# Kernel optimization log

Hardware: AMD Instinct MI355X
Metric: run time of the kernel (lower is better)

The kernel has to match this reference:

```python
import jax, jax.numpy as jnp
import numpy as np

NUM_CLASSES = 1000
FEATURE_DIM = 1024
BATCH = 8192
MOMENTUM = 0.9
LAMBDA_INTRA = 1.0
LAMBDA_INTER = 0.5


def setup_inputs() -> dict:
    key = jax.random.key(0)
    k1, k2, k3, k4 = jax.random.split(key, 4)
    return {
        "features": jax.random.normal(k1, (BATCH, FEATURE_DIM), jnp.float32),
        "features_adv": jax.random.normal(k2, (BATCH, FEATURE_DIM), jnp.float32),
        "centers": jax.random.normal(k3, (NUM_CLASSES, FEATURE_DIM), jnp.float32),
        "labels": jax.random.randint(k4, (BATCH,), 0, NUM_CLASSES, dtype=jnp.int64),
    }


def _l2_normalize(x):
    # torch F.normalize(p=2, dim=1) with eps=1e-12 clamp on the norm
    n = jnp.linalg.norm(x, axis=1, keepdims=True)
    return x / jnp.maximum(n, 1e-12)


def _update_centers(centers, feats, labels):
    # Vectorized version of the per-class masked-mean momentum update.
    C = centers.shape[0]
    sums = jax.ops.segment_sum(feats, labels, num_segments=C)            # [C, D]
    counts = jax.ops.segment_sum(jnp.ones((feats.shape[0],), feats.dtype), labels, num_segments=C)  # [C]
    means = sums / jnp.maximum(counts, 1.0)[:, None]
    has_samples = (counts > 0)[:, None]
    center_is_zero = jnp.all(centers == 0, axis=1, keepdims=True)
    updated = jnp.where(center_is_zero, means, MOMENTUM * centers + (1.0 - MOMENTUM) * means)
    return jnp.where(has_samples, updated, centers)


def reference(features, features_adv, centers, labels):
    f = _l2_normalize(features)
    fa = _l2_normalize(features_adv)

    # update_centers runs under no_grad on detached normalized features
    centers_new = _update_centers(centers, jax.lax.stop_gradient(f), labels)

    centers_batch = centers_new[labels]  # [B, D] gather
    intra_clean = jnp.linalg.norm(f - centers_batch, axis=1).mean()
    intra_adv = jnp.linalg.norm(fa - centers_batch, axis=1).mean()

    # fused pairwise center distances: ||ci||^2 + ||cj||^2 - 2 ci.cj
    sq = jnp.sum(centers_new * centers_new, axis=1)                      # [C]
    d2 = sq[:, None] + sq[None, :] - 2.0 * (centers_new @ centers_new.T)  # [C, C]
    dist = jnp.sqrt(jnp.maximum(d2, 0.0))
    C = centers_new.shape[0]
    upper = jnp.triu(jnp.ones((C, C), dtype=bool), k=1)
    n_pairs = C * (C - 1) / 2.0
    inter_loss = jnp.sum(jnp.where(upper, jax.nn.relu(1.0 - dist), 0.0)) / n_pairs

    return LAMBDA_INTRA * (intra_clean + intra_adv) - LAMBDA_INTER * inter_loss
```

## Files before the change

### kernel.cpp

```cpp
#include <hip/hip_runtime.h>
#include <math.h>

#define BATCH 8192
#define DIM 1024
#define NCLS 1000
#define NPAD 1024
#define NPAIRS 499500.0f

typedef float  f32x4  __attribute__((ext_vector_type(4)));
typedef short  bf16x8 __attribute__((ext_vector_type(8)));


__device__ inline float waveAllReduceAdd(float x) {
  #pragma unroll
  for (int m = 32; m > 0; m >>= 1) x += __shfl_xor(x, m);
  return x;
}

__device__ inline float blockReduce1(float x, float* sm) {
  x = waveAllReduceAdd(x);
  int lane = threadIdx.x & 63, wid = threadIdx.x >> 6;
  __syncthreads();
  if (lane == 0) sm[wid] = x;
  __syncthreads();
  return sm[0] + sm[1] + sm[2] + sm[3];
}

__device__ inline float bf2f(unsigned short u) {
  return __uint_as_float(((unsigned int)u) << 16);
}

__device__ inline unsigned short f2bf(float f) {
  unsigned int u = __float_as_uint(f);
  u += 0x7FFFu + ((u >> 16) & 1u);
  return (unsigned short)(u >> 16);
}


__global__ void zero_kernel(int* counts, float* partials) {
  int t = threadIdx.x;
  if (t < NCLS) counts[t] = 0;
  if (t < 768) partials[t] = 0.0f;
}

__global__ void norms_count_kernel(const float* __restrict__ feats,
                                   const int* __restrict__ labels,
                                   float* __restrict__ invn, int* counts) {
  int lane = threadIdx.x & 63;
  int row = blockIdx.x * 4 + (threadIdx.x >> 6);
  const float4* f4 = (const float4*)(feats + (size_t)row * DIM);
  float ss = 0.f;
  #pragma unroll
  for (int i = 0; i < 4; ++i) {
    float4 v = f4[lane + 64 * i];
    ss += v.x * v.x + v.y * v.y + v.z * v.z + v.w * v.w;
  }
  ss = waveAllReduceAdd(ss);
  if (lane == 0) {
    invn[row] = 1.0f / fmaxf(sqrtf(ss), 1e-12f);
    atomicAdd(&counts[labels[row]], 1);
  }
}

__global__ void scan_kernel(const int* __restrict__ counts, int* offsets, int* cursor) {
  __shared__ int s[1024];
  int t = threadIdx.x;
  int v = (t < NCLS) ? counts[t] : 0;
  s[t] = v;
  __syncthreads();
  for (int off = 1; off < 1024; off <<= 1) {
    int u = (t >= off) ? s[t - off] : 0;
    __syncthreads();
    s[t] += u;
    __syncthreads();
  }
  if (t < NCLS) {
    int e = s[t] - v;
    offsets[t] = e;
    cursor[t] = e;
  }
}

__global__ void scatter_kernel(const int* __restrict__ labels, int* cursor,
                               int* rows_sorted) {
  int j = blockIdx.x * 256 + threadIdx.x;
  if (j < BATCH) {
    int pos = atomicAdd(&cursor[labels[j]], 1);
    rows_sorted[pos] = j;
  }
}


__global__ void update_centers_kernel(const float* __restrict__ feats,
                                      const float* __restrict__ centers,
                                      const int* __restrict__ counts,
                                      const int* __restrict__ offsets,
                                      const int* __restrict__ rows_sorted,
                                      const float* __restrict__ invn,
                                      unsigned short* __restrict__ centers_bf,
                                      float* __restrict__ sqn) {
  __shared__ float sm[8];
  __shared__ int s_anynz;
  int c = blockIdx.x;
  int tid = threadIdx.x;

  if (c >= NCLS) {
    ushort4 z = make_ushort4(0, 0, 0, 0);
    ((ushort4*)(centers_bf + (size_t)c * DIM))[tid] = z;
    return;
  }

  int n = counts[c];
  int off = offsets[c];

  float4 acc = make_float4(0.f, 0.f, 0.f, 0.f);
  for (int t = 0; t < n; ++t) {
    int r = rows_sorted[off + t];
    float w = invn[r];
    float4 v = ((const float4*)(feats + (size_t)r * DIM))[tid];
    acc.x += v.x * w; acc.y += v.y * w; acc.z += v.z * w; acc.w += v.w * w;
  }

  float invc = 1.0f / fmaxf((float)n, 1.0f);
  float4 mean = make_float4(acc.x * invc, acc.y * invc, acc.z * invc, acc.w * invc);

  float4 cv = ((const float4*)(centers + (size_t)c * DIM))[tid];
  if (tid == 0) s_anynz = 0;
  __syncthreads();
  if (cv.x != 0.f || cv.y != 0.f || cv.z != 0.f || cv.w != 0.f) s_anynz = 1;
  __syncthreads();

  float4 o;
  if (s_anynz) {
    o = make_float4(0.9f * cv.x + 0.1f * mean.x, 0.9f * cv.y + 0.1f * mean.y,
                    0.9f * cv.z + 0.1f * mean.z, 0.9f * cv.w + 0.1f * mean.w);
  } else {
    o = mean;
  }
  if (n == 0) o = cv;

  ushort4 ob = make_ushort4(f2bf(o.x), f2bf(o.y), f2bf(o.z), f2bf(o.w));
  ((ushort4*)(centers_bf + (size_t)c * DIM))[tid] = ob;

  float sq = blockReduce1(o.x * o.x + o.y * o.y + o.z * o.z + o.w * o.w, sm);
  if (tid == 0) sqn[c] = sq;
}


__global__ void intra_kernel(const float* __restrict__ feats,
                             const float* __restrict__ featsa,
                             const unsigned short* __restrict__ centers_bf,
                             const int* __restrict__ labels,
                             const float* __restrict__ invn,
                             float* __restrict__ partials) {
  int lane = threadIdx.x & 63;
  int row = blockIdx.x * 4 + (threadIdx.x >> 6);
  const float4* f4 = (const float4*)(feats + (size_t)row * DIM);
  const float4* a4 = (const float4*)(featsa + (size_t)row * DIM);
  int lab = labels[row];
  const ushort4* c4 = (const ushort4*)(centers_bf + (size_t)lab * DIM);

  float4 fv[4], av[4];
  ushort4 cv[4];
  float ssa = 0.f;
  #pragma unroll
  for (int i = 0; i < 4; ++i) {
    fv[i] = f4[lane + 64 * i];
    av[i] = a4[lane + 64 * i];
    cv[i] = c4[lane + 64 * i];
    ssa += av[i].x * av[i].x + av[i].y * av[i].y + av[i].z * av[i].z + av[i].w * av[i].w;
  }
  ssa = waveAllReduceAdd(ssa);
  float inva = 1.0f / fmaxf(sqrtf(ssa), 1e-12f);
  float invf = invn[row];

  float d2c = 0.f, d2a = 0.f;
  #pragma unroll
  for (int i = 0; i < 4; ++i) {
    float cx = bf2f(cv[i].x), cy = bf2f(cv[i].y), cz = bf2f(cv[i].z), cw = bf2f(cv[i].w);
    float dx = fv[i].x * invf - cx, dy = fv[i].y * invf - cy;
    float dz = fv[i].z * invf - cz, dw = fv[i].w * invf - cw;
    d2c += dx * dx + dy * dy + dz * dz + dw * dw;
    float ex = av[i].x * inva - cx, ey = av[i].y * inva - cy;
    float ez = av[i].z * inva - cz, ew = av[i].w * inva - cw;
    d2a += ex * ex + ey * ey + ez * ez + ew * ew;
  }
  d2c = waveAllReduceAdd(d2c);
  d2a = waveAllReduceAdd(d2a);
  if (lane == 0) {
    int slot = row & 255;
    atomicAdd(&partials[slot], sqrtf(d2c));
    atomicAdd(&partials[256 + slot], sqrtf(d2a));
  }
}


__global__ void inter_mfma_kernel(const unsigned short* __restrict__ Cbf,
                                  const float* __restrict__ sq,
                                  float* __restrict__ inter_partial) {
  int bi = blockIdx.y, bj = blockIdx.x;
  if (bj < bi) return;

  __shared__ float smr[8];
  int tid = threadIdx.x;
  int w = tid >> 6;
  int wy = w >> 1, wx = w & 1;
  int lane = tid & 63;
  int m = lane & 15;
  int q = lane >> 4;

  int i0 = bi * 64 + wy * 32;
  int j0 = bj * 64 + wx * 32;

  const unsigned short* arow0 = Cbf + (size_t)(i0 + m) * DIM;
  const unsigned short* arow1 = Cbf + (size_t)(i0 + 16 + m) * DIM;
  const unsigned short* brow0 = Cbf + (size_t)(j0 + m) * DIM;
  const unsigned short* brow1 = Cbf + (size_t)(j0 + 16 + m) * DIM;

  f32x4 acc00 = {0.f, 0.f, 0.f, 0.f}, acc01 = acc00, acc10 = acc00, acc11 = acc00;

  #pragma unroll 4
  for (int k0 = 0; k0 < DIM; k0 += 32) {
    int ko = k0 + q * 8;
    bf16x8 a0 = *(const bf16x8*)(arow0 + ko);
    bf16x8 a1 = *(const bf16x8*)(arow1 + ko);
    bf16x8 b0 = *(const bf16x8*)(brow0 + ko);
    bf16x8 b1 = *(const bf16x8*)(brow1 + ko);
    acc00 = __builtin_amdgcn_mfma_f32_16x16x32_bf16(a0, b0, acc00, 0, 0, 0);
    acc01 = __builtin_amdgcn_mfma_f32_16x16x32_bf16(a0, b1, acc01, 0, 0, 0);
    acc10 = __builtin_amdgcn_mfma_f32_16x16x32_bf16(a1, b0, acc10, 0, 0, 0);
    acc11 = __builtin_amdgcn_mfma_f32_16x16x32_bf16(a1, b1, acc11, 0, 0, 0);
  }

  float local = 0.f;
  int colA = lane & 15;
  int rbase = (lane >> 4) * 4;
  #pragma unroll
  for (int si = 0; si < 2; ++si) {
    #pragma unroll
    for (int sj = 0; sj < 2; ++sj) {
      f32x4 a = (si == 0) ? (sj == 0 ? acc00 : acc01) : (sj == 0 ? acc10 : acc11);
      #pragma unroll
      for (int r = 0; r < 4; ++r) {
        int i = i0 + si * 16 + rbase + r;
        int j = j0 + sj * 16 + colA;
        if (j < NCLS && i < j) {
          float d2 = sq[i] + sq[j] - 2.0f * a[r];
          float d = sqrtf(fmaxf(d2, 0.0f));
          local += fmaxf(1.0f - d, 0.0f);
        }
      }
    }
  }
  float tot = blockReduce1(local, smr);
  if (tid == 0) atomicAdd(&inter_partial[(bi * 16 + bj) & 255], tot);
}


__global__ void final_kernel(const float* __restrict__ partials, float* __restrict__ out) {
  __shared__ float sm[8];
  int t = threadIdx.x;
  float c = partials[t] + partials[256 + t];
  float e = partials[512 + t];
  c = blockReduce1(c, sm);
  e = blockReduce1(e, sm);
  if (t == 0) {
    float intra = c * (1.0f / (float)BATCH);
    float inter = e / NPAIRS;
    out[0] = intra - 0.5f * inter;
  }
}


extern "C" void kernel_launch(void* const* d_in, const int* in_sizes, int n_in,
                              void* d_out, int out_size, void* d_ws, size_t ws_size,
                              hipStream_t stream) {
  const float* features     = (const float*)d_in[0];
  const float* features_adv = (const float*)d_in[1];
  const float* centers      = (const float*)d_in[2];
  const int*   labels       = (const int*)d_in[3];
  float* out = (float*)d_out;

  unsigned short* centers_bf = (unsigned short*)d_ws;
  float* sqn = (float*)(centers_bf + (size_t)NPAD * DIM);
  float* invn = sqn + NCLS;
  float* partials = invn + BATCH;
  int* counts = (int*)(partials + 768);
  int* offsets = counts + NCLS;
  int* cursor = offsets + NCLS;
  int* rows_sorted = cursor + NCLS;

  hipLaunchKernelGGL(zero_kernel, dim3(1), dim3(1024), 0, stream, counts, partials);
  hipLaunchKernelGGL(norms_count_kernel, dim3(BATCH / 4), dim3(256), 0, stream,
                     features, labels, invn, counts);
  hipLaunchKernelGGL(scan_kernel, dim3(1), dim3(1024), 0, stream, counts, offsets, cursor);
  hipLaunchKernelGGL(scatter_kernel, dim3(BATCH / 256), dim3(256), 0, stream, labels,
                     cursor, rows_sorted);
  hipLaunchKernelGGL(update_centers_kernel, dim3(NPAD), dim3(256), 0, stream, features,
                     centers, counts, offsets, rows_sorted, invn, centers_bf, sqn);
  hipLaunchKernelGGL(intra_kernel, dim3(BATCH / 4), dim3(256), 0, stream, features,
                     features_adv, centers_bf, labels, invn, partials);
  hipLaunchKernelGGL(inter_mfma_kernel, dim3(16, 16), dim3(256), 0, stream, centers_bf,
                     sqn, partials + 512);
  hipLaunchKernelGGL(final_kernel, dim3(1), dim3(256), 0, stream, partials, out);
}
```

Measured before the change: 155.1 us.

## Fuse intra-class distance into per-class center update and merge histogram with scan

Merges the zero, label-count and prefix-scan kernels into a single block that builds the histogram in shared memory. The intra-distance kernel is folded into the per-class update kernel: each class block re-reads its samples' clean and adversarial rows and computes distances against the fp32 updated center kept in registers. This removes two launches and the bf16 center gather, but each class block now walks its samples serially with three block-wide reductions (several barriers) per sample. The fused phase also runs at per-class granularity over 1000 blocks, so load imbalance across classes is possible.

```diff
diff --git a/kernel.cpp b/kernel.cpp
--- a/kernel.cpp
+++ b/kernel.cpp
@@ -26,6 +26,16 @@
   return sm[0] + sm[1] + sm[2] + sm[3];
 }
 
+__device__ inline float2 blockReduce2(float x, float y, float* sm) {
+  x = waveAllReduceAdd(x);
+  y = waveAllReduceAdd(y);
+  int lane = threadIdx.x & 63, wid = threadIdx.x >> 6;
+  __syncthreads();
+  if (lane == 0) { sm[wid * 2] = x; sm[wid * 2 + 1] = y; }
+  __syncthreads();
+  return make_float2(sm[0] + sm[2] + sm[4] + sm[6], sm[1] + sm[3] + sm[5] + sm[7]);
+}
+
 __device__ inline float bf2f(unsigned short u) {
   return __uint_as_float(((unsigned int)u) << 16);
 }
@@ -37,15 +47,7 @@
 }
 
 
-__global__ void zero_kernel(int* counts, float* partials) {
-  int t = threadIdx.x;
-  if (t < NCLS) counts[t] = 0;
-  if (t < 768) partials[t] = 0.0f;
-}
-
-__global__ void norms_count_kernel(const float* __restrict__ feats,
-                                   const int* __restrict__ labels,
-                                   float* __restrict__ invn, int* counts) {
+__global__ void norms_kernel(const float* __restrict__ feats, float* __restrict__ invn) {
   int lane = threadIdx.x & 63;
   int row = blockIdx.x * 4 + (threadIdx.x >> 6);
   const float4* f4 = (const float4*)(feats + (size_t)row * DIM);
@@ -56,30 +58,35 @@
     ss += v.x * v.x + v.y * v.y + v.z * v.z + v.w * v.w;
   }
   ss = waveAllReduceAdd(ss);
-  if (lane == 0) {
-    invn[row] = 1.0f / fmaxf(sqrtf(ss), 1e-12f);
-    atomicAdd(&counts[labels[row]], 1);
-  }
-}
-
-__global__ void scan_kernel(const int* __restrict__ counts, int* offsets, int* cursor) {
-  __shared__ int s[1024];
+  if (lane == 0) invn[row] = 1.0f / fmaxf(sqrtf(ss), 1e-12f);
+}
+
+
+__global__ void hist_scan_kernel(const int* __restrict__ labels, int* counts,
+                                 int* offsets, int* cursor, float* partials) {
+  __shared__ int h[1024];
   int t = threadIdx.x;
-  int v = (t < NCLS) ? counts[t] : 0;
-  s[t] = v;
-  __syncthreads();
+  h[t] = 0;
+  if (t < 768) partials[t] = 0.0f;
+  __syncthreads();
+  #pragma unroll
+  for (int j = t; j < BATCH; j += 1024) atomicAdd(&h[labels[j]], 1);
+  __syncthreads();
+  int v = h[t];
+  if (t < NCLS) counts[t] = v;
   for (int off = 1; off < 1024; off <<= 1) {
-    int u = (t >= off) ? s[t - off] : 0;
+    int u = (t >= off) ? h[t - off] : 0;
     __syncthreads();
-    s[t] += u;
+    h[t] += u;
     __syncthreads();
   }
   if (t < NCLS) {
-    int e = s[t] - v;
+    int e = h[t] - v;
     offsets[t] = e;
     cursor[t] = e;
   }
 }
+
 
 __global__ void scatter_kernel(const int* __restrict__ labels, int* cursor,
                                int* rows_sorted) {
@@ -91,22 +98,23 @@
 }
 
 
-__global__ void update_centers_kernel(const float* __restrict__ feats,
-                                      const float* __restrict__ centers,
-                                      const int* __restrict__ counts,
-                                      const int* __restrict__ offsets,
-                                      const int* __restrict__ rows_sorted,
-                                      const float* __restrict__ invn,
-                                      unsigned short* __restrict__ centers_bf,
-                                      float* __restrict__ sqn) {
+__global__ void update_intra_kernel(const float* __restrict__ feats,
+                                    const float* __restrict__ featsa,
+                                    const float* __restrict__ centers,
+                                    const int* __restrict__ counts,
+                                    const int* __restrict__ offsets,
+                                    const int* __restrict__ rows_sorted,
+                                    const float* __restrict__ invn,
+                                    unsigned short* __restrict__ centers_bf,
+                                    float* __restrict__ sqn,
+                                    float* __restrict__ partials) {
   __shared__ float sm[8];
   __shared__ int s_anynz;
   int c = blockIdx.x;
   int tid = threadIdx.x;
 
   if (c >= NCLS) {
-    ushort4 z = make_ushort4(0, 0, 0, 0);
-    ((ushort4*)(centers_bf + (size_t)c * DIM))[tid] = z;
+    ((ushort4*)(centers_bf + (size_t)c * DIM))[tid] = make_ushort4(0, 0, 0, 0);
     return;
   }
 
@@ -120,7 +128,6 @@
     float4 v = ((const float4*)(feats + (size_t)r * DIM))[tid];
     acc.x += v.x * w; acc.y += v.y * w; acc.z += v.z * w; acc.w += v.w * w;
   }
-
   float invc = 1.0f / fmaxf((float)n, 1.0f);
   float4 mean = make_float4(acc.x * invc, acc.y * invc, acc.z * invc, acc.w * invc);
 
@@ -139,58 +146,33 @@
   }
   if (n == 0) o = cv;
 
-  ushort4 ob = make_ushort4(f2bf(o.x), f2bf(o.y), f2bf(o.z), f2bf(o.w));
-  ((ushort4*)(centers_bf + (size_t)c * DIM))[tid] = ob;
+  ((ushort4*)(centers_bf + (size_t)c * DIM))[tid] =
+      make_ushort4(f2bf(o.x), f2bf(o.y), f2bf(o.z), f2bf(o.w));
 
   float sq = blockReduce1(o.x * o.x + o.y * o.y + o.z * o.z + o.w * o.w, sm);
   if (tid == 0) sqn[c] = sq;
-}
-
-
-__global__ void intra_kernel(const float* __restrict__ feats,
-                             const float* __restrict__ featsa,
-                             const unsigned short* __restrict__ centers_bf,
-                             const int* __restrict__ labels,
-                             const float* __restrict__ invn,
-                             float* __restrict__ partials) {
-  int lane = threadIdx.x & 63;
-  int row = blockIdx.x * 4 + (threadIdx.x >> 6);
-  const float4* f4 = (const float4*)(feats + (size_t)row * DIM);
-  const float4* a4 = (const float4*)(featsa + (size_t)row * DIM);
-  int lab = labels[row];
-  const ushort4* c4 = (const ushort4*)(centers_bf + (size_t)lab * DIM);
-
-  float4 fv[4], av[4];
-  ushort4 cv[4];
-  float ssa = 0.f;
-  #pragma unroll
-  for (int i = 0; i < 4; ++i) {
-    fv[i] = f4[lane + 64 * i];
-    av[i] = a4[lane + 64 * i];
-    cv[i] = c4[lane + 64 * i];
-    ssa += av[i].x * av[i].x + av[i].y * av[i].y + av[i].z * av[i].z + av[i].w * av[i].w;
-  }
-  ssa = waveAllReduceAdd(ssa);
-  float inva = 1.0f / fmaxf(sqrtf(ssa), 1e-12f);
-  float invf = invn[row];
-
-  float d2c = 0.f, d2a = 0.f;
-  #pragma unroll
-  for (int i = 0; i < 4; ++i) {
-    float cx = bf2f(cv[i].x), cy = bf2f(cv[i].y), cz = bf2f(cv[i].z), cw = bf2f(cv[i].w);
-    float dx = fv[i].x * invf - cx, dy = fv[i].y * invf - cy;
-    float dz = fv[i].z * invf - cz, dw = fv[i].w * invf - cw;
-    d2c += dx * dx + dy * dy + dz * dz + dw * dw;
-    float ex = av[i].x * inva - cx, ey = av[i].y * inva - cy;
-    float ez = av[i].z * inva - cz, ew = av[i].w * inva - cw;
-    d2a += ex * ex + ey * ey + ez * ez + ew * ew;
-  }
-  d2c = waveAllReduceAdd(d2c);
-  d2a = waveAllReduceAdd(d2a);
-  if (lane == 0) {
-    int slot = row & 255;
-    atomicAdd(&partials[slot], sqrtf(d2c));
-    atomicAdd(&partials[256 + slot], sqrtf(d2a));
+
+  float accC = 0.f, accA = 0.f;
+  for (int t = 0; t < n; ++t) {
+    int r = rows_sorted[off + t];
+    float4 f = ((const float4*)(feats + (size_t)r * DIM))[tid];
+    float4 fa = ((const float4*)(featsa + (size_t)r * DIM))[tid];
+    float ssa = blockReduce1(
+        fa.x * fa.x + fa.y * fa.y + fa.z * fa.z + fa.w * fa.w, sm);
+    float inva = 1.0f / fmaxf(sqrtf(ssa), 1e-12f);
+    float invf = invn[r];
+    float dx = f.x * invf - o.x, dy = f.y * invf - o.y;
+    float dz = f.z * invf - o.z, dw = f.w * invf - o.w;
+    float ex = fa.x * inva - o.x, ey = fa.y * inva - o.y;
+    float ez = fa.z * inva - o.z, ew = fa.w * inva - o.w;
+    float2 d2 = blockReduce2(dx * dx + dy * dy + dz * dz + dw * dw,
+                             ex * ex + ey * ey + ez * ez + ew * ew, sm);
+    if (tid == 0) { accC += sqrtf(d2.x); accA += sqrtf(d2.y); }
+  }
+  if (tid == 0 && n > 0) {
+    int slot = c & 255;
+    atomicAdd(&partials[slot], accC);
+    atomicAdd(&partials[256 + slot], accA);
   }
 }
 
@@ -290,16 +272,15 @@
   int* cursor = offsets + NCLS;
   int* rows_sorted = cursor + NCLS;
 
-  hipLaunchKernelGGL(zero_kernel, dim3(1), dim3(1024), 0, stream, counts, partials);
-  hipLaunchKernelGGL(norms_count_kernel, dim3(BATCH / 4), dim3(256), 0, stream,
-                     features, labels, invn, counts);
-  hipLaunchKernelGGL(scan_kernel, dim3(1), dim3(1024), 0, stream, counts, offsets, cursor);
+  hipLaunchKernelGGL(norms_kernel, dim3(BATCH / 4), dim3(256), 0, stream,
+                     features, invn);
+  hipLaunchKernelGGL(hist_scan_kernel, dim3(1), dim3(1024), 0, stream, labels,
+                     counts, offsets, cursor, partials);
   hipLaunchKernelGGL(scatter_kernel, dim3(BATCH / 256), dim3(256), 0, stream, labels,
                      cursor, rows_sorted);
-  hipLaunchKernelGGL(update_centers_kernel, dim3(NPAD), dim3(256), 0, stream, features,
-                     centers, counts, offsets, rows_sorted, invn, centers_bf, sqn);
-  hipLaunchKernelGGL(intra_kernel, dim3(BATCH / 4), dim3(256), 0, stream, features,
-                     features_adv, centers_bf, labels, invn, partials);
+  hipLaunchKernelGGL(update_intra_kernel, dim3(NPAD), dim3(256), 0, stream, features,
+                     features_adv, centers, counts, offsets, rows_sorted, invn,
+                     centers_bf, sqn, partials);
   hipLaunchKernelGGL(inter_mfma_kernel, dim3(16, 16), dim3(256), 0, stream, centers_bf,
                      sqn, partials + 512);
   hipLaunchKernelGGL(final_kernel, dim3(1), dim3(256), 0, stream, partials, out);
```

New measurement: 161.5 us. 1.04x slower.
